# Kernel optimization log

Measured on AMD Instinct MI355X. Metric: run time of the kernel, lower is better.

## Reference

```python
import jax, jax.numpy as jnp
import numpy as np

N_NODES = 50000
N_EDGES = 640000
IN_FEATS = 512
HID = 128
OUT_FEATS = 128
N_GRAPHS = 256


def setup_inputs() -> dict:
    key = jax.random.key(0)
    ks = jax.random.split(key, 7)
    x = jax.random.normal(ks[0], (N_NODES, IN_FEATS), dtype=jnp.float32)
    edge_index = jax.random.randint(ks[1], (2, N_EDGES), 0, N_NODES, dtype=jnp.int32)
    batch = jnp.sort(jax.random.randint(ks[2], (N_NODES,), 0, N_GRAPHS, dtype=jnp.int32))
    W1 = jax.random.normal(ks[3], (IN_FEATS, HID), dtype=jnp.float32) * (1.0 / np.sqrt(IN_FEATS))
    b1 = jnp.zeros((HID,), jnp.float32)
    W2 = jax.random.normal(ks[4], (HID, OUT_FEATS), dtype=jnp.float32) * (1.0 / np.sqrt(HID))
    b2 = jnp.zeros((OUT_FEATS,), jnp.float32)
    return {"x": x, "W1": W1, "b1": b1, "W2": W2, "b2": b2,
            "edge_index": edge_index, "batch": batch}


def reference(x, W1, b1, W2, b2, edge_index, batch):
    N = x.shape[0]
    loop = jnp.arange(N, dtype=edge_index.dtype)
    # PyG GCNConv default: add self-loops, symmetric deg^-1/2 normalization
    row = jnp.concatenate([edge_index[0], loop])  # source
    col = jnp.concatenate([edge_index[1], loop])  # target
    deg = jax.ops.segment_sum(jnp.ones_like(col, x.dtype), col, num_segments=N)
    dinv = jnp.where(deg > 0, jax.lax.rsqrt(deg), 0.0)
    norm = dinv[row] * dinv[col]  # [E+N]

    def gcn_conv(h, W, b):
        h = h @ W  # linear transform first (PyG order)
        msg = h[row] * norm[:, None]  # gather + scale
        agg = jax.ops.segment_sum(msg, col, num_segments=N)  # scatter-add
        return agg + b

    h = jax.nn.relu(gcn_conv(x, W1, b1))  # dropout is identity in eval mode
    h = gcn_conv(h, W2, b2)
    hs = jax.ops.segment_sum(h, batch, num_segments=N_GRAPHS)  # global_add_pool
    return hs, h
```

## Files before the change

### kernel.cpp

```cpp
#include <hip/hip_runtime.h>
#include <hip/hip_bf16.h>

#define N_NODES  50000
#define N_EDGES  640000
#define IN_FEATS 512
#define HID      128
#define OUT_FEATS 128
#define N_GRAPHS 256

#define SCAN_CHUNK 1024
#define SCAN_BLOCKS ((N_NODES + SCAN_CHUNK - 1) / SCAN_CHUNK)

typedef __attribute__((ext_vector_type(8))) short short8;
typedef __attribute__((ext_vector_type(4))) float f32x4;

__device__ __forceinline__ float bf2f(unsigned u16) {
    return __uint_as_float(u16 << 16);
}
__device__ __forceinline__ unsigned short f2bf(float f) {
    __hip_bfloat16 h = __float2bfloat16(f);
    return *(unsigned short*)&h;
}

#define PREP_BLOCKS 644

__global__ __launch_bounds__(256) void k_prep(const float* __restrict__ W1,
                                              const float* __restrict__ W2,
                                              unsigned short* __restrict__ wt1,
                                              unsigned short* __restrict__ wt2,
                                              int* __restrict__ cnt,
                                              float* __restrict__ hs) {
    int b = blockIdx.x;
    int t = threadIdx.x;
    if (b < 196) {
        int i = b * 256 + t;
        if (i < N_NODES) cnt[i] = 0;
    } else if (b < 452) {
        int idx = (b - 196) * 256 + t;
        int n = idx & 127, k = idx >> 7;
        wt1[(size_t)n * IN_FEATS + k] = f2bf(W1[(size_t)k * 128 + n]);
    } else if (b < 516) {
        int idx = (b - 452) * 256 + t;
        int n = idx & 127, k = idx >> 7;
        wt2[(size_t)n * HID + k] = f2bf(W2[(size_t)k * 128 + n]);
    } else {
        int idx = (b - 516) * 256 + t;
        hs[idx] = 0.f;
    }
}


template <int K>
__global__ __launch_bounds__(256) void k_g1c(const float* __restrict__ A,
                                             const unsigned short* __restrict__ Bt,
                                             unsigned short* __restrict__ Cb, int M,
                                             const int* __restrict__ col,
                                             int* __restrict__ cnt, int nblk_gemm) {
    __shared__ unsigned short As[4][128][8];
    __shared__ unsigned short Bs[4][128][8];
    int tid = threadIdx.x;

    if (blockIdx.x >= nblk_gemm) {
        int e4 = ((blockIdx.x - nblk_gemm) * 256 + tid) * 4;
        if (e4 < N_EDGES) {
            int4 c = *(const int4*)(col + e4);
            atomicAdd(&cnt[c.x], 1);
            atomicAdd(&cnt[c.y], 1);
            atomicAdd(&cnt[c.z], 1);
            atomicAdd(&cnt[c.w], 1);
        }
        return;
    }

    int wave = tid >> 6;
    int lane = tid & 63;
    int quad = lane >> 4;
    int l15 = lane & 15;
    int m0 = blockIdx.x * 128;
    int mw = (wave >> 1) * 64;
    int nw = (wave & 1) * 64;

    f32x4 acc[4][4];
#pragma unroll
    for (int i = 0; i < 4; ++i)
#pragma unroll
        for (int j = 0; j < 4; ++j) acc[i][j] = (f32x4){0.f, 0.f, 0.f, 0.f};

    int r0s = tid >> 2, kq0 = tid & 3;
    int r1s = r0s + 64;
    int gm0 = m0 + r0s; if (gm0 >= M) gm0 = M - 1;
    int gm1 = m0 + r1s; if (gm1 >= M) gm1 = M - 1;
    const float* ap0 = A + (size_t)gm0 * K + kq0 * 8;
    const float* ap1 = A + (size_t)gm1 * K + kq0 * 8;

    for (int k0 = 0; k0 < K; k0 += 32) {
        {
            float4 v0 = *(const float4*)(ap0 + k0);
            float4 v1 = *(const float4*)(ap0 + k0 + 4);
            float f[8] = {v0.x, v0.y, v0.z, v0.w, v1.x, v1.y, v1.z, v1.w};
            short8 pk;
#pragma unroll
            for (int j = 0; j < 8; ++j) pk[j] = (short)f2bf(f[j]);
            *(short8*)&As[kq0][r0s][0] = pk;
            v0 = *(const float4*)(ap1 + k0);
            v1 = *(const float4*)(ap1 + k0 + 4);
            float g[8] = {v0.x, v0.y, v0.z, v0.w, v1.x, v1.y, v1.z, v1.w};
#pragma unroll
            for (int j = 0; j < 8; ++j) pk[j] = (short)f2bf(g[j]);
            *(short8*)&As[kq0][r1s][0] = pk;
        }
#pragma unroll
        for (int i = 0; i < 2; ++i) {
            int slot = tid + i * 256;
            int n = slot >> 2, kq = slot & 3;
            *(short8*)&Bs[kq][n][0] = *(const short8*)(Bt + (size_t)n * K + k0 + kq * 8);
        }
        __syncthreads();
        short8 af[4], bfr[4];
#pragma unroll
        for (int i = 0; i < 4; ++i) af[i] = *(short8*)&As[quad][mw + i * 16 + l15][0];
#pragma unroll
        for (int j = 0; j < 4; ++j) bfr[j] = *(short8*)&Bs[quad][nw + j * 16 + l15][0];
#pragma unroll
        for (int i = 0; i < 4; ++i)
#pragma unroll
            for (int j = 0; j < 4; ++j)
                acc[i][j] = __builtin_amdgcn_mfma_f32_16x16x32_bf16(af[i], bfr[j], acc[i][j], 0, 0, 0);
        __syncthreads();
    }
#pragma unroll
    for (int i = 0; i < 4; ++i) {
        int rb = m0 + mw + i * 16 + quad * 4;
#pragma unroll
        for (int j = 0; j < 4; ++j) {
            int colb = nw + j * 16 + l15;
#pragma unroll
            for (int r2 = 0; r2 < 4; ++r2) {
                int gm = rb + r2;
                if (gm < M) Cb[(size_t)gm * 128 + colb] = f2bf(acc[i][j][r2]);
            }
        }
    }
}


__global__ __launch_bounds__(256) void k_scan_a(const int* __restrict__ cnt,
                                                int* __restrict__ offs,
                                                int* __restrict__ bsum) {
    __shared__ int sums[256];
    int t = threadIdx.x;
    int base = blockIdx.x * SCAN_CHUNK + t * 4;
    int c0 = 0, c1 = 0, c2 = 0, c3 = 0;
    if (base + 3 < N_NODES) {
        int4 v = *(const int4*)(cnt + base);
        c0 = v.x; c1 = v.y; c2 = v.z; c3 = v.w;
    } else {
        if (base + 0 < N_NODES) c0 = cnt[base + 0];
        if (base + 1 < N_NODES) c1 = cnt[base + 1];
        if (base + 2 < N_NODES) c2 = cnt[base + 2];
    }
    int ts = c0 + c1 + c2 + c3;
    sums[t] = ts;
    __syncthreads();
#pragma unroll
    for (int off = 1; off < 256; off <<= 1) {
        int add = (t >= off) ? sums[t - off] : 0;
        __syncthreads();
        sums[t] += add;
        __syncthreads();
    }
    int ex = sums[t] - ts;
    if (base + 3 < N_NODES) {
        int4 o;
        o.x = ex; o.y = ex + c0; o.z = ex + c0 + c1; o.w = ex + c0 + c1 + c2;
        *(int4*)(offs + base) = o;
    } else {
        if (base + 0 < N_NODES) offs[base + 0] = ex;
        if (base + 1 < N_NODES) offs[base + 1] = ex + c0;
        if (base + 2 < N_NODES) offs[base + 2] = ex + c0 + c1;
    }
    if (t == 255) bsum[blockIdx.x] = sums[255];
}

__global__ __launch_bounds__(256) void k_scan_c(const int* __restrict__ cnt,
                                                const int* __restrict__ bsum,
                                                int* __restrict__ offs,
                                                int* __restrict__ cursor,
                                                float* __restrict__ dinv) {
    __shared__ int sb[64];
    int t = threadIdx.x;
    int b = blockIdx.x;
    if (t < 64) sb[t] = (t < SCAN_BLOCKS) ? bsum[t] : 0;
    __syncthreads();
#pragma unroll
    for (int off = 1; off < 64; off <<= 1) {
        int add = 0;
        if (t < 64 && t >= off) add = sb[t - off];
        __syncthreads();
        if (t < 64) sb[t] += add;
        __syncthreads();
    }
    int add = (b == 0) ? 0 : sb[b - 1];
    int base = b * SCAN_CHUNK + t * 4;
    if (base + 3 < N_NODES) {
        int4 o = *(const int4*)(offs + base);
        o.x += add; o.y += add; o.z += add; o.w += add;
        *(int4*)(offs + base) = o;
        *(int4*)(cursor + base) = o;
        int4 c = *(const int4*)(cnt + base);
        float4 d;
        d.x = rsqrtf((float)c.x + 1.0f);
        d.y = rsqrtf((float)c.y + 1.0f);
        d.z = rsqrtf((float)c.z + 1.0f);
        d.w = rsqrtf((float)c.w + 1.0f);
        *(float4*)(dinv + base) = d;
    } else {
#pragma unroll
        for (int j = 0; j < 4; ++j) {
            int i = base + j;
            if (i < N_NODES) {
                int o = offs[i] + add;
                offs[i] = o; cursor[i] = o;
                dinv[i] = rsqrtf((float)cnt[i] + 1.0f);
            }
        }
    }
    if (b == 0 && t == 0) offs[N_NODES] = N_EDGES;
}

__global__ void k_fill(const int* __restrict__ row, const int* __restrict__ col,
                       int* __restrict__ cursor, int* __restrict__ srcIdx) {
    int e4 = (blockIdx.x * blockDim.x + threadIdx.x) * 4;
    if (e4 >= N_EDGES) return;
    int4 r = *(const int4*)(row + e4);
    int4 c = *(const int4*)(col + e4);
    srcIdx[atomicAdd(&cursor[c.x], 1)] = r.x;
    srcIdx[atomicAdd(&cursor[c.y], 1)] = r.y;
    srcIdx[atomicAdd(&cursor[c.z], 1)] = r.z;
    srcIdx[atomicAdd(&cursor[c.w], 1)] = r.w;
}


template <int RELU>
__global__ __launch_bounds__(256) void k_agg(const unsigned* __restrict__ t,
                                             const int* __restrict__ offs,
                                             const int* __restrict__ srcIdx,
                                             const float* __restrict__ dinv,
                                             const float* __restrict__ bias,
                                             unsigned* __restrict__ out_) {
    int wave = threadIdx.x >> 6;
    int lane = threadIdx.x & 63;
    int h = lane >> 5;
    int l = lane & 31;
    int i = blockIdx.x * 4 + wave;
    float di = dinv[i];
    const unsigned* my = t + (size_t)i * 64 + 2 * l;

    float s0 = 0.f, s1 = 0.f, s2 = 0.f, s3 = 0.f;
    {
        uint2 sv = *(const uint2*)my;
        if (h == 0) {
            s0 = bf2f(sv.x & 0xffffu) * di;
            s1 = bf2f(sv.x >> 16) * di;
            s2 = bf2f(sv.y & 0xffffu) * di;
            s3 = bf2f(sv.y >> 16) * di;
        }
    }
    int lo = offs[i], hi = offs[i + 1];
    for (int e = lo; e < hi; e += 16) {
        int idx[8];
        float d[8];
        uint2 v[8];
#pragma unroll
        for (int j = 0; j < 8; ++j) {
            int ee = e + 2 * j + h;
            idx[j] = (ee < hi) ? srcIdx[ee] : i;
        }
#pragma unroll
        for (int j = 0; j < 8; ++j)
            v[j] = *(const uint2*)(t + (size_t)idx[j] * 64 + 2 * l);
#pragma unroll
        for (int j = 0; j < 8; ++j) {
            int ee = e + 2 * j + h;
            d[j] = (ee < hi) ? dinv[idx[j]] : 0.f;
        }
#pragma unroll
        for (int j = 0; j < 8; ++j) {
            s0 = fmaf(bf2f(v[j].x & 0xffffu), d[j], s0);
            s1 = fmaf(bf2f(v[j].x >> 16),     d[j], s1);
            s2 = fmaf(bf2f(v[j].y & 0xffffu), d[j], s2);
            s3 = fmaf(bf2f(v[j].y >> 16),     d[j], s3);
        }
    }
    s0 += __shfl_xor(s0, 32);
    s1 += __shfl_xor(s1, 32);
    s2 += __shfl_xor(s2, 32);
    s3 += __shfl_xor(s3, 32);

    float r0 = s0 * di, r1 = s1 * di, r2 = s2 * di, r3 = s3 * di;
    if (bias) {
        float4 bb = *(const float4*)(bias + 4 * l);
        r0 += bb.x; r1 += bb.y; r2 += bb.z; r3 += bb.w;
    }
    if (RELU) {
        r0 = fmaxf(r0, 0.f); r1 = fmaxf(r1, 0.f);
        r2 = fmaxf(r2, 0.f); r3 = fmaxf(r3, 0.f);
    }
    if (h == 0) {
        uint2 o;
        o.x = (unsigned)f2bf(r0) | ((unsigned)f2bf(r1) << 16);
        o.y = (unsigned)f2bf(r2) | ((unsigned)f2bf(r3) << 16);
        *(uint2*)(out_ + (size_t)i * 64 + 2 * l) = o;
    }
}


__global__ __launch_bounds__(256) void k_gemm2_pool(const unsigned short* __restrict__ G,
                                                    const unsigned short* __restrict__ Bt,
                                                    const float* __restrict__ bias,
                                                    const int* __restrict__ batch,
                                                    float* __restrict__ out,
                                                    float* __restrict__ hs, int M) {
    const int K = HID;
    __shared__ unsigned short As[4][64][8];
    __shared__ unsigned short Bs[4][128][8];
    int tid = threadIdx.x;
    int wave = tid >> 6;
    int lane = tid & 63;
    int quad = lane >> 4;
    int l15 = lane & 15;
    int m0 = blockIdx.x * 64;

    f32x4 acc[8];
#pragma unroll
    for (int nt = 0; nt < 8; ++nt) acc[nt] = (f32x4){0.f, 0.f, 0.f, 0.f};

    int gm_a = m0 + lane; if (gm_a >= M) gm_a = M - 1;
    const unsigned short* ap_base = G + (size_t)gm_a * K + wave * 8;

    for (int k0 = 0; k0 < K; k0 += 32) {
        *(short8*)&As[wave][lane][0] = *(const short8*)(ap_base + k0);
#pragma unroll
        for (int i = 0; i < 2; ++i) {
            int slot = tid + i * 256;
            int bkq = slot >> 7;
            int n = slot & 127;
            *(short8*)&Bs[bkq][n][0] = *(const short8*)(Bt + (size_t)n * K + k0 + bkq * 8);
        }
        __syncthreads();
        short8 a = *(short8*)&As[quad][wave * 16 + l15][0];
#pragma unroll
        for (int nt = 0; nt < 8; ++nt) {
            short8 b = *(short8*)&Bs[quad][nt * 16 + l15][0];
            acc[nt] = __builtin_amdgcn_mfma_f32_16x16x32_bf16(a, b, acc[nt], 0, 0, 0);
        }
        __syncthreads();
    }
    int rb = m0 + wave * 16 + quad * 4;
    int g_[4];
#pragma unroll
    for (int r2 = 0; r2 < 4; ++r2)
        g_[r2] = (rb + r2 < M) ? batch[rb + r2] : -1;
#pragma unroll
    for (int nt = 0; nt < 8; ++nt) {
        int colb = nt * 16 + l15;
        float bcol = bias[colb];
        float v[4];
#pragma unroll
        for (int r2 = 0; r2 < 4; ++r2) {
            v[r2] = acc[nt][r2] + bcol;
            if (rb + r2 < M) out[(size_t)(rb + r2) * 128 + colb] = v[r2];
        }
        float run = v[0];
        int gcur = g_[0];
#pragma unroll
        for (int r2 = 1; r2 < 4; ++r2) {
            if (g_[r2] == gcur) run += v[r2];
            else {
                if (gcur >= 0) atomicAdd(&hs[(size_t)gcur * 128 + colb], run);
                gcur = g_[r2]; run = v[r2];
            }
        }
        if (gcur >= 0) atomicAdd(&hs[(size_t)gcur * 128 + colb], run);
    }
}


extern "C" void kernel_launch(void* const* d_in, const int* in_sizes, int n_in,
                              void* d_out, int out_size, void* d_ws, size_t ws_size,
                              hipStream_t stream) {
    const float* x  = (const float*)d_in[0];
    const float* W1 = (const float*)d_in[1];
    const float* b1 = (const float*)d_in[2];
    const float* W2 = (const float*)d_in[3];
    const float* b2 = (const float*)d_in[4];
    const int*   ei = (const int*)d_in[5];
    const int*   batch = (const int*)d_in[6];
    const int* row = ei;
    const int* col = ei + N_EDGES;

    float* out_hs = (float*)d_out;
    float* out_h  = (float*)d_out + N_GRAPHS * OUT_FEATS;

    char* ws = (char*)d_ws;
    unsigned short* tb   = (unsigned short*)ws;
    unsigned short* h1b  = (unsigned short*)(ws + 12800000);
    unsigned short* gb   = (unsigned short*)(ws + 25600000);
    float* dinv = (float*)(ws + 38400000);
    int*   cnt    = (int*)(ws + 38600000);
    int*   offs   = (int*)(ws + 38800000);
    int*   cursor = (int*)(ws + 39000016);
    int*   srcIdx = (int*)(ws + 39200016);
    int*   bsum   = (int*)(ws + 41761056);
    unsigned short* wt1 = (unsigned short*)(ws + 41761472);
    unsigned short* wt2 = (unsigned short*)(ws + 41892544);

    const int TB = 256;
    const int GB1 = (N_NODES + 127) / 128;
    const int CB  = (N_EDGES / 4 + TB - 1) / TB;

    k_prep<<<PREP_BLOCKS, 256, 0, stream>>>(W1, W2, wt1, wt2, cnt, out_hs);
    k_g1c<IN_FEATS><<<GB1 + CB, 256, 0, stream>>>(x, wt1, tb, N_NODES, col, cnt, GB1);
    k_scan_a<<<SCAN_BLOCKS, 256, 0, stream>>>(cnt, offs, bsum);
    k_scan_c<<<SCAN_BLOCKS, 256, 0, stream>>>(cnt, bsum, offs, cursor, dinv);
    k_fill<<<(N_EDGES / 4 + TB - 1) / TB, TB, 0, stream>>>(row, col, cursor, srcIdx);

    k_agg<1><<<N_NODES / 4, 256, 0, stream>>>((const unsigned*)tb, offs, srcIdx, dinv, b1, (unsigned*)h1b);
    k_agg<0><<<N_NODES / 4, 256, 0, stream>>>((const unsigned*)h1b, offs, srcIdx, dinv, nullptr, (unsigned*)gb);
    k_gemm2_pool<<<(N_NODES + 63) / 64, 256, 0, stream>>>(gb, wt2, b2, batch, out_h, out_hs, N_NODES);
}
```

Measured before the change: 326.0 us.

## Rewrite first GEMM as LDS-free per-wave MFMA with register prefetch

The first-layer GEMM no longer stages tiles through shared memory or uses block barriers. Each wave now computes a 16x128 output strip, loading A (converted fp32 to bf16 in registers) and B fragments straight from global memory, and prefetches the next K-slice into registers while the current MFMAs run. Blocks shrink to 64 rows, giving twice as many, with a launch bound requesting 3 blocks per CU. The trade-off is less on-chip reuse of B: every wave re-reads the whole bf16 weight matrix from cache, and the global load pattern for A is less coalesced.

```diff
diff --git a/kernel.cpp b/kernel.cpp
--- a/kernel.cpp
+++ b/kernel.cpp
@@ -51,13 +51,11 @@
 
 
 template <int K>
-__global__ __launch_bounds__(256) void k_g1c(const float* __restrict__ A,
-                                             const unsigned short* __restrict__ Bt,
-                                             unsigned short* __restrict__ Cb, int M,
-                                             const int* __restrict__ col,
-                                             int* __restrict__ cnt, int nblk_gemm) {
-    __shared__ unsigned short As[4][128][8];
-    __shared__ unsigned short Bs[4][128][8];
+__global__ __launch_bounds__(256, 3) void k_g1c(const float* __restrict__ A,
+                                                const unsigned short* __restrict__ Bt,
+                                                unsigned short* __restrict__ Cb, int M,
+                                                const int* __restrict__ col,
+                                                int* __restrict__ cnt, int nblk_gemm) {
     int tid = threadIdx.x;
 
     if (blockIdx.x >= nblk_gemm) {
@@ -76,69 +74,64 @@
     int lane = tid & 63;
     int quad = lane >> 4;
     int l15 = lane & 15;
-    int m0 = blockIdx.x * 128;
-    int mw = (wave >> 1) * 64;
-    int nw = (wave & 1) * 64;
-
-    f32x4 acc[4][4];
-#pragma unroll
-    for (int i = 0; i < 4; ++i)
-#pragma unroll
-        for (int j = 0; j < 4; ++j) acc[i][j] = (f32x4){0.f, 0.f, 0.f, 0.f};
-
-    int r0s = tid >> 2, kq0 = tid & 3;
-    int r1s = r0s + 64;
-    int gm0 = m0 + r0s; if (gm0 >= M) gm0 = M - 1;
-    int gm1 = m0 + r1s; if (gm1 >= M) gm1 = M - 1;
-    const float* ap0 = A + (size_t)gm0 * K + kq0 * 8;
-    const float* ap1 = A + (size_t)gm1 * K + kq0 * 8;
-
-    for (int k0 = 0; k0 < K; k0 += 32) {
-        {
-            float4 v0 = *(const float4*)(ap0 + k0);
-            float4 v1 = *(const float4*)(ap0 + k0 + 4);
-            float f[8] = {v0.x, v0.y, v0.z, v0.w, v1.x, v1.y, v1.z, v1.w};
-            short8 pk;
-#pragma unroll
-            for (int j = 0; j < 8; ++j) pk[j] = (short)f2bf(f[j]);
-            *(short8*)&As[kq0][r0s][0] = pk;
-            v0 = *(const float4*)(ap1 + k0);
-            v1 = *(const float4*)(ap1 + k0 + 4);
-            float g[8] = {v0.x, v0.y, v0.z, v0.w, v1.x, v1.y, v1.z, v1.w};
-#pragma unroll
-            for (int j = 0; j < 8; ++j) pk[j] = (short)f2bf(g[j]);
-            *(short8*)&As[kq0][r1s][0] = pk;
-        }
-#pragma unroll
-        for (int i = 0; i < 2; ++i) {
-            int slot = tid + i * 256;
-            int n = slot >> 2, kq = slot & 3;
-            *(short8*)&Bs[kq][n][0] = *(const short8*)(Bt + (size_t)n * K + k0 + kq * 8);
-        }
-        __syncthreads();
-        short8 af[4], bfr[4];
-#pragma unroll
-        for (int i = 0; i < 4; ++i) af[i] = *(short8*)&As[quad][mw + i * 16 + l15][0];
-#pragma unroll
-        for (int j = 0; j < 4; ++j) bfr[j] = *(short8*)&Bs[quad][nw + j * 16 + l15][0];
-#pragma unroll
-        for (int i = 0; i < 4; ++i)
-#pragma unroll
-            for (int j = 0; j < 4; ++j)
-                acc[i][j] = __builtin_amdgcn_mfma_f32_16x16x32_bf16(af[i], bfr[j], acc[i][j], 0, 0, 0);
-        __syncthreads();
-    }
-#pragma unroll
-    for (int i = 0; i < 4; ++i) {
-        int rb = m0 + mw + i * 16 + quad * 4;
-#pragma unroll
-        for (int j = 0; j < 4; ++j) {
-            int colb = nw + j * 16 + l15;
-#pragma unroll
-            for (int r2 = 0; r2 < 4; ++r2) {
-                int gm = rb + r2;
-                if (gm < M) Cb[(size_t)gm * 128 + colb] = f2bf(acc[i][j][r2]);
-            }
+    int m0 = blockIdx.x * 64 + wave * 16;
+
+    int row = m0 + l15;
+    if (row >= M) row = M - 1;
+    const float* ap = A + (size_t)row * K + quad * 8;
+    const unsigned short* bp = Bt + (size_t)l15 * K + quad * 8;
+
+    f32x4 acc[8];
+#pragma unroll
+    for (int nt = 0; nt < 8; ++nt) acc[nt] = (f32x4){0.f, 0.f, 0.f, 0.f};
+
+    float4 a0 = *(const float4*)(ap);
+    float4 a1 = *(const float4*)(ap + 4);
+    short8 bcur[8];
+#pragma unroll
+    for (int nt = 0; nt < 8; ++nt)
+        bcur[nt] = *(const short8*)(bp + (size_t)nt * 16 * K);
+
+#pragma unroll 1
+    for (int k0 = 0; k0 < K - 32; k0 += 32) {
+        float4 na0 = *(const float4*)(ap + k0 + 32);
+        float4 na1 = *(const float4*)(ap + k0 + 36);
+        short8 bn[8];
+#pragma unroll
+        for (int nt = 0; nt < 8; ++nt)
+            bn[nt] = *(const short8*)(bp + (size_t)nt * 16 * K + k0 + 32);
+
+        short8 af;
+        af[0] = (short)f2bf(a0.x); af[1] = (short)f2bf(a0.y);
+        af[2] = (short)f2bf(a0.z); af[3] = (short)f2bf(a0.w);
+        af[4] = (short)f2bf(a1.x); af[5] = (short)f2bf(a1.y);
+        af[6] = (short)f2bf(a1.z); af[7] = (short)f2bf(a1.w);
+#pragma unroll
+        for (int nt = 0; nt < 8; ++nt)
+            acc[nt] = __builtin_amdgcn_mfma_f32_16x16x32_bf16(af, bcur[nt], acc[nt], 0, 0, 0);
+
+        a0 = na0; a1 = na1;
+#pragma unroll
+        for (int nt = 0; nt < 8; ++nt) bcur[nt] = bn[nt];
+    }
+    {
+        short8 af;
+        af[0] = (short)f2bf(a0.x); af[1] = (short)f2bf(a0.y);
+        af[2] = (short)f2bf(a0.z); af[3] = (short)f2bf(a0.w);
+        af[4] = (short)f2bf(a1.x); af[5] = (short)f2bf(a1.y);
+        af[6] = (short)f2bf(a1.z); af[7] = (short)f2bf(a1.w);
+#pragma unroll
+        for (int nt = 0; nt < 8; ++nt)
+            acc[nt] = __builtin_amdgcn_mfma_f32_16x16x32_bf16(af, bcur[nt], acc[nt], 0, 0, 0);
+    }
+
+#pragma unroll
+    for (int nt = 0; nt < 8; ++nt) {
+        int colb = nt * 16 + l15;
+#pragma unroll
+        for (int r2 = 0; r2 < 4; ++r2) {
+            int gm = m0 + quad * 4 + r2;
+            if (gm < M) Cb[(size_t)gm * 128 + colb] = f2bf(acc[nt][r2]);
         }
     }
 }
@@ -416,7 +409,7 @@
     unsigned short* wt2 = (unsigned short*)(ws + 41892544);
 
     const int TB = 256;
-    const int GB1 = (N_NODES + 127) / 128;
+    const int GB1 = (N_NODES + 63) / 64;
     const int CB  = (N_EDGES / 4 + TB - 1) / TB;
 
     k_prep<<<PREP_BLOCKS, 256, 0, stream>>>(W1, W2, wt1, wt2, cnt, out_hs);
```

Result: slower. 351.6 us (+7.8%).

## Double-buffer GEMM1 with direct global-to-LDS loads and smaller M tiles

Applied to the files above, without the earlier changes.

Restructures the first GEMM so fp32 A tiles and bf16 B tiles are copied straight into LDS with global_load_lds, double-buffered with prefetch two k-steps ahead and explicit vmcnt waits. The fp32-to-bf16 conversion moves from the staging path to after the LDS read. The M tile shrinks from 128 to 64 rows per block, doubling the block count, and launch bounds request higher occupancy. The goal is to hide global-load latency behind MFMA work. The cost is more B-tile reloads per output row, larger fp32 LDS traffic, and manual waitcnt bookkeeping that must match the issued load count.

```diff
diff --git a/kernel.cpp b/kernel.cpp
--- a/kernel.cpp
+++ b/kernel.cpp
@@ -20,6 +20,21 @@
 __device__ __forceinline__ unsigned short f2bf(float f) {
     __hip_bfloat16 h = __float2bfloat16(f);
     return *(unsigned short*)&h;
+}
+
+__device__ __forceinline__ short8 cvt8(float4 x, float4 y) {
+    short8 r;
+    r[0] = (short)f2bf(x.x); r[1] = (short)f2bf(x.y);
+    r[2] = (short)f2bf(x.z); r[3] = (short)f2bf(x.w);
+    r[4] = (short)f2bf(y.x); r[5] = (short)f2bf(y.y);
+    r[6] = (short)f2bf(y.z); r[7] = (short)f2bf(y.w);
+    return r;
+}
+
+__device__ __forceinline__ void gl_lds16(const void* g, void* l) {
+    __builtin_amdgcn_global_load_lds(
+        (const __attribute__((address_space(1))) void*)g,
+        (__attribute__((address_space(3))) void*)l, 16, 0, 0);
 }
 
 #define PREP_BLOCKS 644
@@ -51,13 +66,13 @@
 
 
 template <int K>
-__global__ __launch_bounds__(256) void k_g1c(const float* __restrict__ A,
-                                             const unsigned short* __restrict__ Bt,
-                                             unsigned short* __restrict__ Cb, int M,
-                                             const int* __restrict__ col,
-                                             int* __restrict__ cnt, int nblk_gemm) {
-    __shared__ unsigned short As[4][128][8];
-    __shared__ unsigned short Bs[4][128][8];
+__global__ __launch_bounds__(256, 4) void k_g1c(const float* __restrict__ A,
+                                                const unsigned short* __restrict__ Bt,
+                                                unsigned short* __restrict__ Cb, int M,
+                                                const int* __restrict__ col,
+                                                int* __restrict__ cnt, int nblk_gemm) {
+    __shared__ float          As[2][2][4][64][4];
+    __shared__ unsigned short Bs[2][4][128][8];
     int tid = threadIdx.x;
 
     if (blockIdx.x >= nblk_gemm) {
@@ -76,64 +91,79 @@
     int lane = tid & 63;
     int quad = lane >> 4;
     int l15 = lane & 15;
-    int m0 = blockIdx.x * 128;
-    int mw = (wave >> 1) * 64;
-    int nw = (wave & 1) * 64;
-
-    f32x4 acc[4][4];
-#pragma unroll
-    for (int i = 0; i < 4; ++i)
+    int wm = wave >> 1;
+    int wn = wave & 1;
+    int m0 = blockIdx.x * 64;
+
+#define STAGE(buf, k0) {                                                        \
+    _Pragma("unroll")                                                           \
+    for (int is = 0; is < 2; ++is) {                                            \
+        int c = (wave * 2 + is) * 64 + lane;                                    \
+        int h = c >> 8, kq = (c >> 6) & 3, r = c & 63;                          \
+        int gr = m0 + r; if (gr >= M) gr = M - 1;                               \
+        const float* g = A + (size_t)gr * K + (k0) + kq * 8 + h * 4;            \
+        void* l = (char*)&As[buf][0][0][0][0] + (wave * 2 + is) * 1024;         \
+        gl_lds16(g, l);                                                         \
+    }                                                                           \
+    _Pragma("unroll")                                                           \
+    for (int is = 0; is < 2; ++is) {                                            \
+        int c = (wave * 2 + is) * 64 + lane;                                    \
+        int kq = c >> 7, r = c & 127;                                           \
+        const unsigned short* g = Bt + (size_t)r * K + (k0) + kq * 8;           \
+        void* l = (char*)&Bs[buf][0][0][0] + (wave * 2 + is) * 1024;            \
+        gl_lds16(g, l);                                                         \
+    }                                                                           \
+}
+
+    f32x4 acc[2][4];
+#pragma unroll
+    for (int i = 0; i < 2; ++i)
 #pragma unroll
         for (int j = 0; j < 4; ++j) acc[i][j] = (f32x4){0.f, 0.f, 0.f, 0.f};
 
-    int r0s = tid >> 2, kq0 = tid & 3;
-    int r1s = r0s + 64;
-    int gm0 = m0 + r0s; if (gm0 >= M) gm0 = M - 1;
-    int gm1 = m0 + r1s; if (gm1 >= M) gm1 = M - 1;
-    const float* ap0 = A + (size_t)gm0 * K + kq0 * 8;
-    const float* ap1 = A + (size_t)gm1 * K + kq0 * 8;
-
-    for (int k0 = 0; k0 < K; k0 += 32) {
-        {
-            float4 v0 = *(const float4*)(ap0 + k0);
-            float4 v1 = *(const float4*)(ap0 + k0 + 4);
-            float f[8] = {v0.x, v0.y, v0.z, v0.w, v1.x, v1.y, v1.z, v1.w};
-            short8 pk;
-#pragma unroll
-            for (int j = 0; j < 8; ++j) pk[j] = (short)f2bf(f[j]);
-            *(short8*)&As[kq0][r0s][0] = pk;
-            v0 = *(const float4*)(ap1 + k0);
-            v1 = *(const float4*)(ap1 + k0 + 4);
-            float g[8] = {v0.x, v0.y, v0.z, v0.w, v1.x, v1.y, v1.z, v1.w};
-#pragma unroll
-            for (int j = 0; j < 8; ++j) pk[j] = (short)f2bf(g[j]);
-            *(short8*)&As[kq0][r1s][0] = pk;
-        }
-#pragma unroll
-        for (int i = 0; i < 2; ++i) {
-            int slot = tid + i * 256;
-            int n = slot >> 2, kq = slot & 3;
-            *(short8*)&Bs[kq][n][0] = *(const short8*)(Bt + (size_t)n * K + k0 + kq * 8);
-        }
-        __syncthreads();
-        short8 af[4], bfr[4];
-#pragma unroll
-        for (int i = 0; i < 4; ++i) af[i] = *(short8*)&As[quad][mw + i * 16 + l15][0];
-#pragma unroll
-        for (int j = 0; j < 4; ++j) bfr[j] = *(short8*)&Bs[quad][nw + j * 16 + l15][0];
-#pragma unroll
-        for (int i = 0; i < 4; ++i)
-#pragma unroll
-            for (int j = 0; j < 4; ++j)
-                acc[i][j] = __builtin_amdgcn_mfma_f32_16x16x32_bf16(af[i], bfr[j], acc[i][j], 0, 0, 0);
-        __syncthreads();
-    }
-#pragma unroll
-    for (int i = 0; i < 4; ++i) {
-        int rb = m0 + mw + i * 16 + quad * 4;
+    const int NT = K / 32;
+    STAGE(0, 0);
+    STAGE(1, 32);
+
+#pragma unroll 1
+    for (int t = 0; t < NT; ++t) {
+        int buf = t & 1;
+        if (t == NT - 1) { asm volatile("s_waitcnt vmcnt(0)" ::: "memory"); }
+        else             { asm volatile("s_waitcnt vmcnt(4)" ::: "memory"); }
+        __builtin_amdgcn_s_barrier();
+
+        float4 lo0 = *(const float4*)&As[buf][0][quad][wm * 32 + l15][0];
+        float4 hi0 = *(const float4*)&As[buf][1][quad][wm * 32 + l15][0];
+        float4 lo1 = *(const float4*)&As[buf][0][quad][wm * 32 + 16 + l15][0];
+        float4 hi1 = *(const float4*)&As[buf][1][quad][wm * 32 + 16 + l15][0];
+        short8 bfr[4];
+#pragma unroll
+        for (int j = 0; j < 4; ++j)
+            bfr[j] = *(const short8*)&Bs[buf][quad][wn * 64 + j * 16 + l15][0];
+
+        asm volatile("s_waitcnt lgkmcnt(0)" ::: "memory");
+        __builtin_amdgcn_sched_barrier(0);
+        __builtin_amdgcn_s_barrier();
+
+        if (t < NT - 2) STAGE(buf, (t + 2) * 32);
+        __builtin_amdgcn_sched_barrier(0);
+
+        short8 a0 = cvt8(lo0, hi0);
+        short8 a1 = cvt8(lo1, hi1);
 #pragma unroll
         for (int j = 0; j < 4; ++j) {
-            int colb = nw + j * 16 + l15;
+            acc[0][j] = __builtin_amdgcn_mfma_f32_16x16x32_bf16(a0, bfr[j], acc[0][j], 0, 0, 0);
+            acc[1][j] = __builtin_amdgcn_mfma_f32_16x16x32_bf16(a1, bfr[j], acc[1][j], 0, 0, 0);
+        }
+    }
+#undef STAGE
+
+#pragma unroll
+    for (int i = 0; i < 2; ++i) {
+        int rb = m0 + wm * 32 + i * 16 + quad * 4;
+#pragma unroll
+        for (int j = 0; j < 4; ++j) {
+            int colb = wn * 64 + j * 16 + l15;
 #pragma unroll
             for (int r2 = 0; r2 < 4; ++r2) {
                 int gm = rb + r2;
@@ -416,7 +446,7 @@
     unsigned short* wt2 = (unsigned short*)(ws + 41892544);
 
     const int TB = 256;
-    const int GB1 = (N_NODES + 127) / 128;
+    const int GB1 = (N_NODES + 63) / 64;
     const int CB  = (N_EDGES / 4 + TB - 1) / TB;
 
     k_prep<<<PREP_BLOCKS, 256, 0, stream>>>(W1, W2, wt1, wt2, cnt, out_hs);
```

Measured after the change: 329.8 us. About the same (+1.2%).
